# Performance work log

Measured on AMD Instinct MI355X. Metric: run time of the kernel, lower is better.

The kernel has to match this reference:

```python
import jax, jax.numpy as jnp
import numpy as np
import math

T, B = 2048, 32
N_CLASSES = 64
D_MODEL = 512
N_LAYERS = 2
N_HEADS = 8
D_HEAD = 64
D_FF = N_HEADS * D_HEAD * 4  # 2048
E_VAL = (D_MODEL + 1) // 2   # 256 value-embedding dim
D_PE = D_MODEL // 2          # 256 positional dim (concatenated)
EPS_ATTN = 1e-6
EPS_LN = 1e-5


def _pe_table(t, d):
    pos = np.arange(t, dtype=np.float32)[:, None]
    div = np.exp(np.arange(0, d, 2, dtype=np.float32) * (-math.log(10000.0) / d))
    pe = np.zeros((t, d), dtype=np.float32)
    pe[:, 0::2] = np.sin(pos * div)
    pe[:, 1::2] = np.cos(pos * div)
    return jnp.asarray(pe)


def _ln(h, g, b):
    m = jnp.mean(h, axis=-1, keepdims=True)
    v = jnp.mean((h - m) ** 2, axis=-1, keepdims=True)
    return (h - m) * jax.lax.rsqrt(v + EPS_LN) * g + b


def setup_inputs() -> dict:
    key = jax.random.key(0)
    ks = jax.random.split(key, 12)
    s = 0.02
    L, dm, dff = N_LAYERS, D_MODEL, D_FF
    return {
        "x": jax.random.randint(ks[0], (T, B), 0, N_CLASSES),
        "E": jax.random.normal(ks[1], (N_CLASSES, E_VAL)) * s,
        "Wq": jax.random.normal(ks[2], (L, dm, dm)) * s, "bq": jnp.zeros((L, dm)),
        "Wk": jax.random.normal(ks[3], (L, dm, dm)) * s, "bk": jnp.zeros((L, dm)),
        "Wv": jax.random.normal(ks[4], (L, dm, dm)) * s, "bv": jnp.zeros((L, dm)),
        "Wo": jax.random.normal(ks[5], (L, dm, dm)) * s, "bo": jnp.zeros((L, dm)),
        "g1": jnp.ones((L, dm)), "be1": jnp.zeros((L, dm)),
        "W1": jax.random.normal(ks[6], (L, dm, dff)) * s, "b1": jnp.zeros((L, dff)),
        "W2": jax.random.normal(ks[7], (L, dff, dm)) * s, "b2": jnp.zeros((L, dm)),
        "g2": jnp.ones((L, dm)), "be2": jnp.zeros((L, dm)),
        "Wp": jax.random.normal(ks[8], (dm, N_CLASSES)) * s, "bp": jnp.zeros((N_CLASSES,)),
    }


def reference(x, E, Wq, bq, Wk, bk, Wv, bv, Wo, bo, g1, be1, W1, b1, W2, b2, g2, be2, Wp, bp):
    # embed tokens: x [T,B] -> [T,B,E_VAL]; concat positional (broadcast over batch) -> [T,B,D_MODEL]
    emb = E[x]
    pe = _pe_table(T, D_PE)
    h0 = jnp.concatenate([emb, jnp.broadcast_to(pe[:, None, :], (T, B, D_PE))], axis=-1)

    Si0 = jnp.zeros((N_LAYERS, B, N_HEADS, D_HEAD, D_HEAD), h0.dtype)  # sum_t k \otimes v
    Zi0 = jnp.zeros((N_LAYERS, B, N_HEADS, D_HEAD), h0.dtype)          # sum_t k

    phi = lambda u: jax.nn.elu(u) + 1.0  # linear-attention feature map

    def step(carry, xt):
        Si, Zi = carry
        h = xt  # [B, D_MODEL]
        for l in range(N_LAYERS):
            q = phi((h @ Wq[l] + bq[l]).reshape(B, N_HEADS, D_HEAD))
            k = phi((h @ Wk[l] + bk[l]).reshape(B, N_HEADS, D_HEAD))
            v = (h @ Wv[l] + bv[l]).reshape(B, N_HEADS, D_HEAD)
            Sl = Si[l] + k[..., :, None] * v[..., None, :]   # [B,H,D,D]
            Zl = Zi[l] + k
            num = jnp.einsum("bhd,bhdm->bhm", q, Sl)
            den = jnp.einsum("bhd,bhd->bh", q, Zl) + EPS_ATTN
            attn = (num / den[..., None]).reshape(B, N_HEADS * D_HEAD) @ Wo[l] + bo[l]
            h = _ln(h + attn, g1[l], be1[l])
            ff = jax.nn.relu(h @ W1[l] + b1[l]) @ W2[l] + b2[l]
            h = _ln(h + ff, g2[l], be2[l])
            Si = Si.at[l].set(Sl)
            Zi = Zi.at[l].set(Zl)
        return (Si, Zi), h

    _, ys = jax.lax.scan(step, (Si0, Zi0), h0)       # [T,B,D_MODEL]
    y_hat = jnp.transpose(ys, (1, 0, 2)) @ Wp + bp   # [B,T,N_CLASSES]
    return y_hat
```

## Files before the change

kernel.cpp:

```cpp
#include <hip/hip_runtime.h>


typedef unsigned short u16;
typedef __bf16 bf16x8 __attribute__((ext_vector_type(8)));
typedef float f32x4 __attribute__((ext_vector_type(4)));

#define T_SEQ 2048
#define BATCH 32
#define NHEADS 8
#define CT 64
#define NCHUNK 32

__device__ __forceinline__ float b2f(u16 u) {
    union { unsigned int i; float f; } v; v.i = ((unsigned int)u) << 16; return v.f;
}
__device__ __forceinline__ u16 f2b(float f) {
    union { float f; unsigned int i; } v; v.f = f;
    unsigned int r = (v.i + 0x7FFFu + ((v.i >> 16) & 1u)) >> 16;
    return (u16)r;
}

__device__ __forceinline__ void gl_lds16(const u16* g, u16* l) {
    __builtin_amdgcn_global_load_lds(
        (const __attribute__((address_space(1))) void*)g,
        (__attribute__((address_space(3))) void*)l,
        16, 0, 0);
}

template<int ACT>
__global__ __launch_bounds__(256) void gemm_mx(
    const u16* __restrict__ A, const u16* __restrict__ BT,
    const float* __restrict__ bias, u16* __restrict__ C,
    int M, int N, int K, int act_split, int nbn, int GM)
{
    __shared__ __align__(16) u16 As[128 * 64];
    __shared__ __align__(16) u16 Bs[128 * 64];

    const int bid = blockIdx.x;
    const int gsz = GM * nbn;
    const int grp = bid / gsz, rm = bid % gsz;
    const int bm = (grp * GM + rm % GM) * 128;
    const int bn = (rm / GM) * 128;

    const int tid = threadIdx.x;
    const int lane = tid & 63;
    const int w = tid >> 6;
    const int lrow = lane & 15, quad = lane >> 4;
    const int wrow = (w >> 1) * 64, wcol = (w & 1) * 64;
    const int sr = lane >> 3;
    const int sg = lane & 7;

    f32x4 acc[4][4] = {};

    for (int k0 = 0; k0 < K; k0 += 64) {
        #pragma unroll
        for (int ch4 = 0; ch4 < 4; ch4++) {
            const int chunk = w * 4 + ch4;
            const int r = chunk * 8 + sr;
            const int gs = sg ^ (r & 7);
            gl_lds16(A  + (size_t)(bm + r) * K + k0 + gs * 8, As + chunk * 512);
            gl_lds16(BT + (size_t)(bn + r) * K + k0 + gs * 8, Bs + chunk * 512);
        }
        __syncthreads();
        #pragma unroll
        for (int half = 0; half < 2; half++) {
            bf16x8 af[4], bfv[4];
            #pragma unroll
            for (int i = 0; i < 4; i++) {
                const int r = wrow + i * 16 + lrow;
                const int gq = (half * 4 + quad) ^ (r & 7);
                af[i] = *(const bf16x8*)&As[r * 64 + gq * 8];
            }
            #pragma unroll
            for (int j = 0; j < 4; j++) {
                const int r = wcol + j * 16 + lrow;
                const int gq = (half * 4 + quad) ^ (r & 7);
                bfv[j] = *(const bf16x8*)&Bs[r * 64 + gq * 8];
            }
            #pragma unroll
            for (int i = 0; i < 4; i++)
                #pragma unroll
                for (int j = 0; j < 4; j++)
                    acc[i][j] = __builtin_amdgcn_mfma_f32_16x16x32_bf16(
                        af[i], bfv[j], acc[i][j], 0, 0, 0);
        }
        __syncthreads();
    }

    #pragma unroll
    for (int i = 0; i < 4; i++) {
        const int row0 = bm + wrow + i * 16 + quad * 4;
        #pragma unroll
        for (int j = 0; j < 4; j++) {
            const int col = bn + wcol + j * 16 + lrow;
            const float bb = bias[col];
            #pragma unroll
            for (int r = 0; r < 4; r++) {
                float v = acc[i][j][r] + bb;
                if (ACT == 1) v = fmaxf(v, 0.f);
                if (ACT == 2) { if (col < act_split) v = (v > 0.f) ? (v + 1.f) : __expf(v); }
                C[(size_t)(row0 + r) * N + col] = f2b(v);
            }
        }
    }
}

template<int BM, int BN, int WM, int WN>
__global__ __launch_bounds__(WM*WN*64) void gemm_sm(
    const u16* __restrict__ A, const u16* __restrict__ BT,
    const float* __restrict__ bias, float* __restrict__ C,
    int M, int N, int K)
{
    constexpr int BK = 32;
    constexpr int LDT = BK + 8;
    constexpr int NTHR = WM * WN * 64;
    __shared__ __align__(16) u16 As[BM * LDT];
    __shared__ __align__(16) u16 Bs[BN * LDT];

    const int tid = threadIdx.x;
    const int bm = blockIdx.y * BM;
    const int bn = blockIdx.x * BN;
    const int lane = tid & 63;
    const int wid = tid >> 6;
    const int wrow = (wid / WN) * (BM / WM);
    const int wcol = (wid % WN) * (BN / WN);
    constexpr int FM = BM / WM / 16;
    constexpr int FN = BN / WN / 16;
    const int lrow = lane & 15;
    const int lk = (lane >> 4) * 8;

    f32x4 acc[FM][FN] = {};

    for (int k0 = 0; k0 < K; k0 += BK) {
        #pragma unroll
        for (int g0 = 0; g0 < BM * 4; g0 += NTHR) {
            int g = g0 + tid;
            int row = g >> 2, kk = (g & 3) * 8;
            *(uint4*)&As[row * LDT + kk] =
                *(const uint4*)&A[(size_t)(bm + row) * K + k0 + kk];
        }
        #pragma unroll
        for (int g0 = 0; g0 < BN * 4; g0 += NTHR) {
            int g = g0 + tid;
            int row = g >> 2, kk = (g & 3) * 8;
            *(uint4*)&Bs[row * LDT + kk] =
                *(const uint4*)&BT[(size_t)(bn + row) * K + k0 + kk];
        }
        __syncthreads();
        bf16x8 af[FM], bfv[FN];
        #pragma unroll
        for (int i = 0; i < FM; i++)
            af[i] = *(const bf16x8*)&As[(wrow + i * 16 + lrow) * LDT + lk];
        #pragma unroll
        for (int j = 0; j < FN; j++)
            bfv[j] = *(const bf16x8*)&Bs[(wcol + j * 16 + lrow) * LDT + lk];
        #pragma unroll
        for (int i = 0; i < FM; i++)
            #pragma unroll
            for (int j = 0; j < FN; j++)
                acc[i][j] = __builtin_amdgcn_mfma_f32_16x16x32_bf16(
                    af[i], bfv[j], acc[i][j], 0, 0, 0);
        __syncthreads();
    }

    #pragma unroll
    for (int i = 0; i < FM; i++) {
        const int row0 = bm + wrow + i * 16 + (lane >> 4) * 4;
        #pragma unroll
        for (int j = 0; j < FN; j++) {
            const int col = bn + wcol + j * 16 + (lane & 15);
            const float bb = bias[col];
            #pragma unroll
            for (int r = 0; r < 4; r++)
                C[(size_t)(row0 + r) * N + col] = acc[i][j][r] + bb;
        }
    }
}

__global__ __launch_bounds__(256) void transpose_w(
    const float* __restrict__ src, u16* __restrict__ dst, int K, int N)
{
    __shared__ float tile[32][33];
    int bx = blockIdx.x, by = blockIdx.y;
    int tx = threadIdx.x & 31, ty = threadIdx.x >> 5;
    #pragma unroll
    for (int yy = 0; yy < 4; yy++) {
        int k = by * 32 + ty + yy * 8;
        tile[ty + yy * 8][tx] = src[(size_t)k * N + bx * 32 + tx];
    }
    __syncthreads();
    #pragma unroll
    for (int yy = 0; yy < 4; yy++) {
        int n = bx * 32 + ty + yy * 8;
        dst[(size_t)n * K + by * 32 + tx] = f2b(tile[tx][ty + yy * 8]);
    }
}

__global__ __launch_bounds__(256) void concat_bias(
    const float* __restrict__ bq, const float* __restrict__ bk,
    const float* __restrict__ bv, float* __restrict__ dst)
{
    int id = blockIdx.x * 256 + threadIdx.x;
    if (id >= 3072) return;
    int l = id / 1536, i = id % 1536;
    float v = (i < 512) ? bq[l * 512 + i]
            : (i < 1024) ? bk[l * 512 + i - 512]
                         : bv[l * 512 + i - 1024];
    dst[id] = v;
}

__global__ __launch_bounds__(256) void embed_kernel(
    const int* __restrict__ x, const float* __restrict__ E, u16* __restrict__ h,
    int b0)
{
    int e = blockIdx.x * 256 + threadIdx.x;
    int r = e >> 9;
    int c = e & 511;
    int t = r & (T_SEQ - 1);
    int b = b0 + (r >> 11);
    float v;
    if (c < 256) {
        v = E[x[t * BATCH + b] * 256 + c];
    } else {
        int j = c - 256;
        int i = j >> 1;
        float div = expf(-(float)(2 * i) * (9.210340371976184f / 256.f));
        float arg = (float)t * div;
        v = (j & 1) ? cosf(arg) : sinf(arg);
    }
    h[e] = f2b(v);
}

__global__ __launch_bounds__(256) void attn_chunk_sums(
    const u16* __restrict__ qkv, u16* __restrict__ S, float* __restrict__ Z,
    int BHg)
{
    __shared__ __align__(16) u16 Kt[64 * 72], Vt[64 * 72];
    int bid = blockIdx.x;
    int bh = bid % BHg, c = bid / BHg;
    int bl = bh >> 3, hh = bh & 7;
    for (int idx = threadIdx.x; idx < 4096; idx += 256) {
        int t = idx >> 6, d = idx & 63;
        size_t r = ((size_t)(bl * T_SEQ + c * 64 + t)) * 1536 + hh * 64 + d;
        Kt[d * 72 + t] = qkv[r + 512];
        Vt[d * 72 + t] = qkv[r + 1024];
    }
    __syncthreads();
    int lane = threadIdx.x & 63;
    int w = threadIdx.x >> 6;
    int lrow = lane & 15, quad = lane >> 4;
    int m0 = w * 16;
    f32x4 acc[4] = {};
    #pragma unroll
    for (int k0 = 0; k0 < 64; k0 += 32) {
        bf16x8 af = *(const bf16x8*)&Vt[(m0 + lrow) * 72 + k0 + quad * 8];
        #pragma unroll
        for (int jt = 0; jt < 4; jt++) {
            bf16x8 bf = *(const bf16x8*)&Kt[(jt * 16 + lrow) * 72 + k0 + quad * 8];
            acc[jt] = __builtin_amdgcn_mfma_f32_16x16x32_bf16(af, bf, acc[jt], 0, 0, 0);
        }
    }
    size_t base = ((size_t)c * BHg + bh) * 4096;
    #pragma unroll
    for (int jt = 0; jt < 4; jt++)
        #pragma unroll
        for (int r = 0; r < 4; r++) {
            int row = m0 + quad * 4 + r;
            int col = jt * 16 + lrow;
            S[base + row * 64 + col] = f2b(acc[jt][r]);
        }
    if (threadIdx.x < 64) {
        float z = 0.f;
        #pragma unroll
        for (int t8 = 0; t8 < 64; t8 += 8) {
            bf16x8 kk = *(const bf16x8*)&Kt[threadIdx.x * 72 + t8];
            #pragma unroll
            for (int u = 0; u < 8; u++) z += (float)kk[u];
        }
        Z[((size_t)c * BHg + bh) * 64 + threadIdx.x] = z;
    }
}

__global__ __launch_bounds__(256) void attn_prefix(
    u16* __restrict__ S, float* __restrict__ Z, int BHg)
{
    int gid = blockIdx.x * 256 + threadIdx.x;
    int bh = gid >> 12, e = gid & 4095;
    size_t stride = (size_t)BHg * 4096;
    size_t base = (size_t)bh * 4096 + e;
    float v[NCHUNK];
    #pragma unroll
    for (int c = 0; c < NCHUNK; c++) v[c] = b2f(S[base + c * stride]);
    float run = 0.f;
    #pragma unroll
    for (int c = 0; c < NCHUNK; c++) {
        float t = v[c]; S[base + c * stride] = f2b(run); run += t;
    }
    if (gid < BHg * 64) {
        size_t zb = (size_t)gid;
        size_t zs = (size_t)BHg * 64;
        float zv[NCHUNK];
        #pragma unroll
        for (int c = 0; c < NCHUNK; c++) zv[c] = Z[zb + c * zs];
        float zr = 0.f;
        #pragma unroll
        for (int c = 0; c < NCHUNK; c++) {
            float t = zv[c]; Z[zb + c * zs] = zr; zr += t;
        }
    }
}

__global__ __launch_bounds__(256) void attn_intra(
    const u16* __restrict__ qkv, const u16* __restrict__ Sp,
    const float* __restrict__ Zp, u16* __restrict__ out, int BHg)
{
    __shared__ __align__(16) u16 Qs[64 * 72], Ks[64 * 72], Vt[64 * 72],
                                 Ps[64 * 72], Ssh[64 * 72];
    __shared__ float Zsh[64], den2sh[64];
    int bid = blockIdx.x;
    int bh = bid % BHg, c = bid / BHg;
    int bl = bh >> 3, hh = bh & 7;
    size_t sbase = ((size_t)c * BHg + bh) * 4096;
    for (int idx = threadIdx.x; idx < 4096; idx += 256) {
        int t = idx >> 6, d = idx & 63;
        size_t r = ((size_t)(bl * T_SEQ + c * 64 + t)) * 1536 + hh * 64 + d;
        Qs[t * 72 + d] = qkv[r];
        Ks[t * 72 + d] = qkv[r + 512];
        Vt[d * 72 + t] = qkv[r + 1024];
        Ssh[t * 72 + d] = Sp[sbase + idx];
    }
    if (threadIdx.x < 64)
        Zsh[threadIdx.x] = Zp[((size_t)c * BHg + bh) * 64 + threadIdx.x];
    __syncthreads();

    if (threadIdx.x < 64) {
        float s = 0.f;
        #pragma unroll
        for (int d8 = 0; d8 < 64; d8 += 8) {
            bf16x8 qq = *(const bf16x8*)&Qs[threadIdx.x * 72 + d8];
            #pragma unroll
            for (int u = 0; u < 8; u++) s += (float)qq[u] * Zsh[d8 + u];
        }
        den2sh[threadIdx.x] = s;
    }

    int lane = threadIdx.x & 63;
    int w = threadIdx.x >> 6;
    int lrow = lane & 15, quad = lane >> 4;
    int i0 = w * 16;

    f32x4 accp[4] = {};
    #pragma unroll
    for (int k0 = 0; k0 < 64; k0 += 32) {
        bf16x8 af = *(const bf16x8*)&Qs[(i0 + lrow) * 72 + k0 + quad * 8];
        #pragma unroll
        for (int jt = 0; jt < 4; jt++) {
            bf16x8 bf = *(const bf16x8*)&Ks[(jt * 16 + lrow) * 72 + k0 + quad * 8];
            accp[jt] = __builtin_amdgcn_mfma_f32_16x16x32_bf16(af, bf, accp[jt], 0, 0, 0);
        }
    }
    float den1[4] = {0.f, 0.f, 0.f, 0.f};
    #pragma unroll
    for (int r = 0; r < 4; r++) {
        int row = i0 + quad * 4 + r;
        #pragma unroll
        for (int jt = 0; jt < 4; jt++) {
            int col = jt * 16 + lrow;
            float pv = (col <= row) ? accp[jt][r] : 0.f;
            den1[r] += pv;
            Ps[row * 72 + col] = f2b(pv);
        }
        #pragma unroll
        for (int off = 1; off < 16; off <<= 1)
            den1[r] += __shfl_xor(den1[r], off, 64);
    }
    __syncthreads();

    f32x4 acco[4] = {};
    #pragma unroll
    for (int k0 = 0; k0 < 64; k0 += 32) {
        bf16x8 af = *(const bf16x8*)&Ps[(i0 + lrow) * 72 + k0 + quad * 8];
        #pragma unroll
        for (int jt = 0; jt < 4; jt++) {
            bf16x8 bf = *(const bf16x8*)&Vt[(jt * 16 + lrow) * 72 + k0 + quad * 8];
            acco[jt] = __builtin_amdgcn_mfma_f32_16x16x32_bf16(af, bf, acco[jt], 0, 0, 0);
        }
    }
    #pragma unroll
    for (int k0 = 0; k0 < 64; k0 += 32) {
        bf16x8 af = *(const bf16x8*)&Qs[(i0 + lrow) * 72 + k0 + quad * 8];
        #pragma unroll
        for (int jt = 0; jt < 4; jt++) {
            bf16x8 bf = *(const bf16x8*)&Ssh[(jt * 16 + lrow) * 72 + k0 + quad * 8];
            acco[jt] = __builtin_amdgcn_mfma_f32_16x16x32_bf16(af, bf, acco[jt], 0, 0, 0);
        }
    }
    #pragma unroll
    for (int r = 0; r < 4; r++) {
        int row = i0 + quad * 4 + r;
        float inv = 1.f / (den1[r] + den2sh[row] + 1e-6f);
        size_t orow = ((size_t)(bl * T_SEQ + c * 64 + row)) * 512 + hh * 64;
        #pragma unroll
        for (int jt = 0; jt < 4; jt++)
            out[orow + jt * 16 + lrow] = f2b(acco[jt][r] * inv);
    }
}

__global__ __launch_bounds__(256) void ln_kernel(
    const u16* h, const u16* delta,
    const float* __restrict__ g, const float* __restrict__ be, u16* out)
{
    int row = blockIdx.x * 4 + (threadIdx.x >> 6);
    int lane = threadIdx.x & 63;
    size_t base = (size_t)row * 512 + lane * 8;
    uint4 hv = *(const uint4*)&h[base];
    uint4 dv = *(const uint4*)&delta[base];
    const u16* hp = (const u16*)&hv;
    const u16* dp = (const u16*)&dv;
    float x[8]; float s = 0.f;
    #pragma unroll
    for (int i = 0; i < 8; i++) { x[i] = b2f(hp[i]) + b2f(dp[i]); s += x[i]; }
    #pragma unroll
    for (int off = 32; off > 0; off >>= 1) s += __shfl_xor(s, off, 64);
    float m = s * (1.f / 512.f);
    float vs = 0.f;
    #pragma unroll
    for (int i = 0; i < 8; i++) { float t = x[i] - m; vs += t * t; }
    #pragma unroll
    for (int off = 32; off > 0; off >>= 1) vs += __shfl_xor(vs, off, 64);
    float rstd = rsqrtf(vs * (1.f / 512.f) + 1e-5f);
    union { u16 u[8]; uint4 v; } o;
    #pragma unroll
    for (int i = 0; i < 8; i++)
        o.u[i] = f2b((x[i] - m) * rstd * g[lane * 8 + i] + be[lane * 8 + i]);
    *(uint4*)&out[base] = o.v;
}

extern "C" void kernel_launch(void* const* d_in, const int* in_sizes, int n_in,
                              void* d_out, int out_size, void* d_ws, size_t ws_size,
                              hipStream_t stream)
{
    const int*   x  = (const int*)d_in[0];
    const float* E  = (const float*)d_in[1];
    const float* Wq = (const float*)d_in[2];
    const float* bq = (const float*)d_in[3];
    const float* Wk = (const float*)d_in[4];
    const float* bk = (const float*)d_in[5];
    const float* Wv = (const float*)d_in[6];
    const float* bv = (const float*)d_in[7];
    const float* Wo = (const float*)d_in[8];
    const float* bo = (const float*)d_in[9];
    const float* g1 = (const float*)d_in[10];
    const float* be1= (const float*)d_in[11];
    const float* W1 = (const float*)d_in[12];
    const float* b1 = (const float*)d_in[13];
    const float* W2 = (const float*)d_in[14];
    const float* b2 = (const float*)d_in[15];
    const float* g2 = (const float*)d_in[16];
    const float* be2= (const float*)d_in[17];
    const float* Wp = (const float*)d_in[18];
    const float* bp = (const float*)d_in[19];

    char* p = (char*)d_ws;
    u16* qkvT = (u16*)p; p += (size_t)2 * 1536 * 512 * 2;
    u16* woT  = (u16*)p; p += (size_t)2 * 512 * 512 * 2;
    u16* w1T  = (u16*)p; p += (size_t)2 * 2048 * 512 * 2;
    u16* w2T  = (u16*)p; p += (size_t)2 * 512 * 2048 * 2;
    u16* wpT  = (u16*)p; p += (size_t)64 * 512 * 2;
    float* bqkv = (float*)p; p += (size_t)16384;
    size_t fixed = (size_t)(p - (char*)d_ws);

    const size_t perB = 12648448ULL;
    int Bg = 32;
    while (Bg > 1 && fixed + (size_t)Bg * perB > ws_size) Bg >>= 1;
    const int rows = Bg * T_SEQ;
    const int BHg = Bg * NHEADS;
    const int nbm = rows / 128;

    u16* h      = (u16*)p; p += (size_t)rows * 512 * 2;
    u16* qkvBig = (u16*)p; p += (size_t)rows * 2048 * 2;
    u16* am     = (u16*)p; p += (size_t)rows * 512 * 2;
    float* Z    = (float*)p; p += (size_t)BHg * NCHUNK * 64 * 4;
    u16* qkv = qkvBig;
    u16* Sb  = qkvBig + (size_t)rows * 1536;
    u16* ff1 = qkvBig;
    u16* o_  = qkvBig;

    dim3 blk(256);

    for (int l = 0; l < 2; l++) {
        transpose_w<<<dim3(16, 16), blk, 0, stream>>>(Wq + (size_t)l * 262144, qkvT + (size_t)l * 786432,          512, 512);
        transpose_w<<<dim3(16, 16), blk, 0, stream>>>(Wk + (size_t)l * 262144, qkvT + (size_t)l * 786432 + 262144, 512, 512);
        transpose_w<<<dim3(16, 16), blk, 0, stream>>>(Wv + (size_t)l * 262144, qkvT + (size_t)l * 786432 + 524288, 512, 512);
        transpose_w<<<dim3(16, 16), blk, 0, stream>>>(Wo + (size_t)l * 262144, woT + (size_t)l * 262144,           512, 512);
        transpose_w<<<dim3(64, 16), blk, 0, stream>>>(W1 + (size_t)l * 1048576, w1T + (size_t)l * 1048576,         512, 2048);
        transpose_w<<<dim3(16, 64), blk, 0, stream>>>(W2 + (size_t)l * 1048576, w2T + (size_t)l * 1048576,         2048, 512);
    }
    transpose_w<<<dim3(2, 16), blk, 0, stream>>>(Wp, wpT, 512, 64);
    concat_bias<<<12, blk, 0, stream>>>(bq, bk, bv, bqkv);

    for (int b0 = 0; b0 < BATCH; b0 += Bg) {
        embed_kernel<<<rows * 2, blk, 0, stream>>>(x, E, h, b0);

        for (int l = 0; l < 2; l++) {
            gemm_mx<2><<<dim3(nbm * 12), blk, 0, stream>>>(
                h, qkvT + (size_t)l * 786432, bqkv + l * 1536, qkv,
                rows, 1536, 512, 1024, 12, 8);
            attn_chunk_sums<<<NCHUNK * BHg, blk, 0, stream>>>(qkv, Sb, Z, BHg);
            attn_prefix<<<BHg * 16, blk, 0, stream>>>(Sb, Z, BHg);
            attn_intra<<<NCHUNK * BHg, blk, 0, stream>>>(qkv, Sb, Z, am, BHg);
            gemm_mx<0><<<dim3(nbm * 4), blk, 0, stream>>>(
                am, woT + (size_t)l * 262144, bo + l * 512, o_,
                rows, 512, 512, 0, 4, 8);
            ln_kernel<<<rows / 4, blk, 0, stream>>>(h, o_, g1 + l * 512, be1 + l * 512, h);
            gemm_mx<1><<<dim3(nbm * 16), blk, 0, stream>>>(
                h, w1T + (size_t)l * 1048576, b1 + l * 2048, ff1,
                rows, 2048, 512, 0, 16, 8);
            gemm_mx<0><<<dim3(nbm * 4), blk, 0, stream>>>(
                ff1, w2T + (size_t)l * 1048576, b2 + l * 512, am,
                rows, 512, 2048, 0, 4, 8);
            ln_kernel<<<rows / 4, blk, 0, stream>>>(h, am, g2 + l * 512, be2 + l * 512, h);
        }

        gemm_sm<64, 64, 2, 2><<<dim3(1, rows / 64), blk, 0, stream>>>(
            h, wpT, bp, (float*)d_out + (size_t)b0 * T_SEQ * 64, rows, 64, 512);
    }

    (void)in_sizes; (void)n_in; (void)out_size; (void)ws_size;
}
```

Baseline: 1.739 ms.

## Swap MFMA operands for vectorized epilogue stores and fuse residual add into GEMM

Swaps the A/B operands of the MFMA calls so that each lane holds four consecutive columns of one row. The GEMM and attention epilogues can then write packed 8-byte (bf16) or 16-byte (fp32) vectors instead of scattered scalar stores, and bias is loaded as a float4. The residual add is moved into the Wo and W2 GEMM epilogues, so the layer-norm kernel reads one tensor instead of two. Also replaces the manual bf16 rounding with a native conversion, and passes the attention denominators through shared memory to match the new output layout.

```diff
diff --git a/kernel.cpp b/kernel.cpp
--- a/kernel.cpp
+++ b/kernel.cpp
@@ -15,9 +15,7 @@
     union { unsigned int i; float f; } v; v.i = ((unsigned int)u) << 16; return v.f;
 }
 __device__ __forceinline__ u16 f2b(float f) {
-    union { float f; unsigned int i; } v; v.f = f;
-    unsigned int r = (v.i + 0x7FFFu + ((v.i >> 16) & 1u)) >> 16;
-    return (u16)r;
+    union { __bf16 b; u16 u; } v; v.b = (__bf16)f; return v.u;
 }
 
 __device__ __forceinline__ void gl_lds16(const u16* g, u16* l) {
@@ -27,10 +25,11 @@
         16, 0, 0);
 }
 
-template<int ACT>
+template<int ACT, bool RES>
 __global__ __launch_bounds__(256) void gemm_mx(
     const u16* __restrict__ A, const u16* __restrict__ BT,
-    const float* __restrict__ bias, u16* __restrict__ C,
+    const float* __restrict__ bias, const u16* __restrict__ R,
+    u16* __restrict__ C,
     int M, int N, int K, int act_split, int nbn, int GM)
 {
     __shared__ __align__(16) u16 As[128 * 64];
@@ -82,25 +81,41 @@
                 #pragma unroll
                 for (int j = 0; j < 4; j++)
                     acc[i][j] = __builtin_amdgcn_mfma_f32_16x16x32_bf16(
-                        af[i], bfv[j], acc[i][j], 0, 0, 0);
+                        bfv[j], af[i], acc[i][j], 0, 0, 0);
         }
         __syncthreads();
     }
 
     #pragma unroll
     for (int i = 0; i < 4; i++) {
-        const int row0 = bm + wrow + i * 16 + quad * 4;
+        const int row = bm + wrow + i * 16 + lrow;
         #pragma unroll
         for (int j = 0; j < 4; j++) {
-            const int col = bn + wcol + j * 16 + lrow;
-            const float bb = bias[col];
-            #pragma unroll
-            for (int r = 0; r < 4; r++) {
-                float v = acc[i][j][r] + bb;
-                if (ACT == 1) v = fmaxf(v, 0.f);
-                if (ACT == 2) { if (col < act_split) v = (v > 0.f) ? (v + 1.f) : __expf(v); }
-                C[(size_t)(row0 + r) * N + col] = f2b(v);
+            const int col0 = bn + wcol + j * 16 + quad * 4;
+            const float4 bb = *(const float4*)&bias[col0];
+            float v[4] = { acc[i][j][0] + bb.x, acc[i][j][1] + bb.y,
+                           acc[i][j][2] + bb.z, acc[i][j][3] + bb.w };
+            if (RES) {
+                uint2 rv = *(const uint2*)&R[(size_t)row * N + col0];
+                const u16* rp = (const u16*)&rv;
+                #pragma unroll
+                for (int r = 0; r < 4; r++) v[r] += b2f(rp[r]);
             }
+            if (ACT == 1) {
+                #pragma unroll
+                for (int r = 0; r < 4; r++) v[r] = fmaxf(v[r], 0.f);
+            }
+            if (ACT == 2) {
+                if (col0 < act_split) {
+                    #pragma unroll
+                    for (int r = 0; r < 4; r++)
+                        v[r] = (v[r] > 0.f) ? (v[r] + 1.f) : __expf(v[r]);
+                }
+            }
+            union { u16 q[4]; uint2 d; } pk;
+            #pragma unroll
+            for (int r = 0; r < 4; r++) pk.q[r] = f2b(v[r]);
+            *(uint2*)&C[(size_t)row * N + col0] = pk.d;
         }
     }
 }
@@ -159,20 +174,20 @@
             #pragma unroll
             for (int j = 0; j < FN; j++)
                 acc[i][j] = __builtin_amdgcn_mfma_f32_16x16x32_bf16(
-                    af[i], bfv[j], acc[i][j], 0, 0, 0);
+                    bfv[j], af[i], acc[i][j], 0, 0, 0);
         __syncthreads();
     }
 
     #pragma unroll
     for (int i = 0; i < FM; i++) {
-        const int row0 = bm + wrow + i * 16 + (lane >> 4) * 4;
+        const int row = bm + wrow + i * 16 + lrow;
         #pragma unroll
         for (int j = 0; j < FN; j++) {
-            const int col = bn + wcol + j * 16 + (lane & 15);
-            const float bb = bias[col];
-            #pragma unroll
-            for (int r = 0; r < 4; r++)
-                C[(size_t)(row0 + r) * N + col] = acc[i][j][r] + bb;
+            const int col0 = bn + wcol + j * 16 + (lane >> 4) * 4;
+            const float4 bb = *(const float4*)&bias[col0];
+            float4 o = { acc[i][j][0] + bb.x, acc[i][j][1] + bb.y,
+                         acc[i][j][2] + bb.z, acc[i][j][3] + bb.w };
+            *(float4*)&C[(size_t)row * N + col0] = o;
         }
     }
 }
@@ -257,18 +272,19 @@
         #pragma unroll
         for (int jt = 0; jt < 4; jt++) {
             bf16x8 bf = *(const bf16x8*)&Kt[(jt * 16 + lrow) * 72 + k0 + quad * 8];
-            acc[jt] = __builtin_amdgcn_mfma_f32_16x16x32_bf16(af, bf, acc[jt], 0, 0, 0);
+            acc[jt] = __builtin_amdgcn_mfma_f32_16x16x32_bf16(bf, af, acc[jt], 0, 0, 0);
         }
     }
     size_t base = ((size_t)c * BHg + bh) * 4096;
-    #pragma unroll
-    for (int jt = 0; jt < 4; jt++)
-        #pragma unroll
-        for (int r = 0; r < 4; r++) {
-            int row = m0 + quad * 4 + r;
-            int col = jt * 16 + lrow;
-            S[base + row * 64 + col] = f2b(acc[jt][r]);
-        }
+    const int m = m0 + lrow;
+    #pragma unroll
+    for (int jt = 0; jt < 4; jt++) {
+        const int d0 = jt * 16 + quad * 4;
+        union { u16 q[4]; uint2 u; } pk;
+        #pragma unroll
+        for (int r = 0; r < 4; r++) pk.q[r] = f2b(acc[jt][r]);
+        *(uint2*)&S[base + m * 64 + d0] = pk.u;
+    }
     if (threadIdx.x < 64) {
         float z = 0.f;
         #pragma unroll
@@ -316,7 +332,7 @@
 {
     __shared__ __align__(16) u16 Qs[64 * 72], Ks[64 * 72], Vt[64 * 72],
                                  Ps[64 * 72], Ssh[64 * 72];
-    __shared__ float Zsh[64], den2sh[64];
+    __shared__ float Zsh[64], den2sh[64], den1sh[64];
     int bid = blockIdx.x;
     int bh = bid % BHg, c = bid / BHg;
     int bl = bh >> 3, hh = bh & 7;
@@ -359,67 +375,68 @@
             accp[jt] = __builtin_amdgcn_mfma_f32_16x16x32_bf16(af, bf, accp[jt], 0, 0, 0);
         }
     }
-    float den1[4] = {0.f, 0.f, 0.f, 0.f};
     #pragma unroll
     for (int r = 0; r < 4; r++) {
         int row = i0 + quad * 4 + r;
+        float d1 = 0.f;
         #pragma unroll
         for (int jt = 0; jt < 4; jt++) {
             int col = jt * 16 + lrow;
             float pv = (col <= row) ? accp[jt][r] : 0.f;
-            den1[r] += pv;
+            d1 += pv;
             Ps[row * 72 + col] = f2b(pv);
         }
         #pragma unroll
         for (int off = 1; off < 16; off <<= 1)
-            den1[r] += __shfl_xor(den1[r], off, 64);
+            d1 += __shfl_xor(d1, off, 64);
+        if (lrow == 0) den1sh[row] = d1;
     }
     __syncthreads();
 
     f32x4 acco[4] = {};
     #pragma unroll
     for (int k0 = 0; k0 < 64; k0 += 32) {
-        bf16x8 af = *(const bf16x8*)&Ps[(i0 + lrow) * 72 + k0 + quad * 8];
+        bf16x8 ps = *(const bf16x8*)&Ps[(i0 + lrow) * 72 + k0 + quad * 8];
         #pragma unroll
         for (int jt = 0; jt < 4; jt++) {
-            bf16x8 bf = *(const bf16x8*)&Vt[(jt * 16 + lrow) * 72 + k0 + quad * 8];
-            acco[jt] = __builtin_amdgcn_mfma_f32_16x16x32_bf16(af, bf, acco[jt], 0, 0, 0);
+            bf16x8 vf = *(const bf16x8*)&Vt[(jt * 16 + lrow) * 72 + k0 + quad * 8];
+            acco[jt] = __builtin_amdgcn_mfma_f32_16x16x32_bf16(vf, ps, acco[jt], 0, 0, 0);
         }
     }
     #pragma unroll
     for (int k0 = 0; k0 < 64; k0 += 32) {
-        bf16x8 af = *(const bf16x8*)&Qs[(i0 + lrow) * 72 + k0 + quad * 8];
+        bf16x8 qf = *(const bf16x8*)&Qs[(i0 + lrow) * 72 + k0 + quad * 8];
         #pragma unroll
         for (int jt = 0; jt < 4; jt++) {
-            bf16x8 bf = *(const bf16x8*)&Ssh[(jt * 16 + lrow) * 72 + k0 + quad * 8];
-            acco[jt] = __builtin_amdgcn_mfma_f32_16x16x32_bf16(af, bf, acco[jt], 0, 0, 0);
-        }
-    }
-    #pragma unroll
-    for (int r = 0; r < 4; r++) {
-        int row = i0 + quad * 4 + r;
-        float inv = 1.f / (den1[r] + den2sh[row] + 1e-6f);
-        size_t orow = ((size_t)(bl * T_SEQ + c * 64 + row)) * 512 + hh * 64;
-        #pragma unroll
-        for (int jt = 0; jt < 4; jt++)
-            out[orow + jt * 16 + lrow] = f2b(acco[jt][r] * inv);
+            bf16x8 sf = *(const bf16x8*)&Ssh[(jt * 16 + lrow) * 72 + k0 + quad * 8];
+            acco[jt] = __builtin_amdgcn_mfma_f32_16x16x32_bf16(sf, qf, acco[jt], 0, 0, 0);
+        }
+    }
+    const int i = i0 + lrow;
+    const float inv = 1.f / (den1sh[i] + den2sh[i] + 1e-6f);
+    size_t orow = ((size_t)(bl * T_SEQ + c * 64 + i)) * 512 + hh * 64;
+    #pragma unroll
+    for (int jt = 0; jt < 4; jt++) {
+        const int m0 = jt * 16 + quad * 4;
+        union { u16 q[4]; uint2 u; } pk;
+        #pragma unroll
+        for (int r = 0; r < 4; r++) pk.q[r] = f2b(acco[jt][r] * inv);
+        *(uint2*)&out[orow + m0] = pk.u;
     }
 }
 
 __global__ __launch_bounds__(256) void ln_kernel(
-    const u16* h, const u16* delta,
-    const float* __restrict__ g, const float* __restrict__ be, u16* out)
+    const u16* __restrict__ s_in,
+    const float* __restrict__ g, const float* __restrict__ be, u16* __restrict__ out)
 {
     int row = blockIdx.x * 4 + (threadIdx.x >> 6);
     int lane = threadIdx.x & 63;
     size_t base = (size_t)row * 512 + lane * 8;
-    uint4 hv = *(const uint4*)&h[base];
-    uint4 dv = *(const uint4*)&delta[base];
+    uint4 hv = *(const uint4*)&s_in[base];
     const u16* hp = (const u16*)&hv;
-    const u16* dp = (const u16*)&dv;
     float x[8]; float s = 0.f;
     #pragma unroll
-    for (int i = 0; i < 8; i++) { x[i] = b2f(hp[i]) + b2f(dp[i]); s += x[i]; }
+    for (int i = 0; i < 8; i++) { x[i] = b2f(hp[i]); s += x[i]; }
     #pragma unroll
     for (int off = 32; off > 0; off >>= 1) s += __shfl_xor(s, off, 64);
     float m = s * (1.f / 512.f);
@@ -503,23 +520,23 @@
         embed_kernel<<<rows * 2, blk, 0, stream>>>(x, E, h, b0);
 
         for (int l = 0; l < 2; l++) {
-            gemm_mx<2><<<dim3(nbm * 12), blk, 0, stream>>>(
-                h, qkvT + (size_t)l * 786432, bqkv + l * 1536, qkv,
+            gemm_mx<2, false><<<dim3(nbm * 12), blk, 0, stream>>>(
+                h, qkvT + (size_t)l * 786432, bqkv + l * 1536, nullptr, qkv,
                 rows, 1536, 512, 1024, 12, 8);
             attn_chunk_sums<<<NCHUNK * BHg, blk, 0, stream>>>(qkv, Sb, Z, BHg);
             attn_prefix<<<BHg * 16, blk, 0, stream>>>(Sb, Z, BHg);
             attn_intra<<<NCHUNK * BHg, blk, 0, stream>>>(qkv, Sb, Z, am, BHg);
-            gemm_mx<0><<<dim3(nbm * 4), blk, 0, stream>>>(
-                am, woT + (size_t)l * 262144, bo + l * 512, o_,
+            gemm_mx<0, true><<<dim3(nbm * 4), blk, 0, stream>>>(
+                am, woT + (size_t)l * 262144, bo + l * 512, h, o_,
                 rows, 512, 512, 0, 4, 8);
-            ln_kernel<<<rows / 4, blk, 0, stream>>>(h, o_, g1 + l * 512, be1 + l * 512, h);
-            gemm_mx<1><<<dim3(nbm * 16), blk, 0, stream>>>(
-                h, w1T + (size_t)l * 1048576, b1 + l * 2048, ff1,
+            ln_kernel<<<rows / 4, blk, 0, stream>>>(o_, g1 + l * 512, be1 + l * 512, h);
+            gemm_mx<1, false><<<dim3(nbm * 16), blk, 0, stream>>>(
+                h, w1T + (size_t)l * 1048576, b1 + l * 2048, nullptr, ff1,
                 rows, 2048, 512, 0, 16, 8);
-            gemm_mx<0><<<dim3(nbm * 4), blk, 0, stream>>>(
-                ff1, w2T + (size_t)l * 1048576, b2 + l * 512, am,
+            gemm_mx<0, true><<<dim3(nbm * 4), blk, 0, stream>>>(
+                ff1, w2T + (size_t)l * 1048576, b2 + l * 512, h, am,
                 rows, 512, 2048, 0, 4, 8);
-            ln_kernel<<<rows / 4, blk, 0, stream>>>(h, am, g2 + l * 512, be2 + l * 512, h);
+            ln_kernel<<<rows / 4, blk, 0, stream>>>(am, g2 + l * 512, be2 + l * 512, h);
         }
 
         gemm_sm<64, 64, 2, 2><<<dim3(1, rows / 64), blk, 0, stream>>>(
```

Result: slower. 1.878 ms (+8.0%).
